# Performance work log

Hardware: AMD Instinct MI355X
Metric: run time of the kernel (lower is better)

The kernel has to match this reference:

```python
import jax, jax.numpy as jnp
import numpy as np


def setup_inputs() -> dict:
    key = jax.random.key(0)
    ks = jax.random.split(key, 7)
    B, S, D, F, E = 4, 2048, 1024, 4096, 8
    scale = 0.02
    return {
        "x": jax.random.normal(ks[0], (B, S, D), dtype=jnp.float32),
        "gate_w": jax.random.normal(ks[1], (D, E), dtype=jnp.float32) * scale,
        "gate_b": jnp.zeros((E,), dtype=jnp.float32),
        "w1": jax.random.normal(ks[2], (E, D, F), dtype=jnp.float32) * scale,
        "b1": jnp.zeros((E, F), dtype=jnp.float32),
        "w2": jax.random.normal(ks[3], (E, F, D), dtype=jnp.float32) * scale,
        "b2": jnp.zeros((E, D), dtype=jnp.float32),
        "top_k": 2,
    }


def reference(x, gate_w, gate_b, w1, b1, w2, b2, top_k):
    B, S, D = x.shape
    E = w1.shape[0]
    xf = x.reshape(-1, D)                      # [T, D], T = B*S
    T = xf.shape[0]

    # Router: top-k logits, softmax over the selected k (as in torch code)
    logits = xf @ gate_w + gate_b              # [T, E]
    rw, sel = jax.lax.top_k(logits, top_k)     # [T, k], [T, k]
    w = jax.nn.softmax(rw, axis=-1)            # [T, k]

    # Dense combine weights: combine[t, e] = sum_k w[t,k] * (sel[t,k]==e)
    combine = jnp.zeros((T, E), dtype=xf.dtype)
    combine = combine.at[jnp.arange(T)[:, None], sel].add(w)

    # Loop over small fixed expert count; each expert FFN on all tokens,
    # weighted by combine (zero for unrouted tokens). Dropout p honored as 0 (eval).
    out = jnp.zeros_like(xf)
    for e in range(E):
        h = jax.nn.gelu(xf @ w1[e] + b1[e], approximate=False)  # torch F.gelu = exact
        out = out + combine[:, e:e + 1] * (h @ w2[e] + b2[e])
    return out.reshape(B, S, D)
```

## Files before the change

### kernel.cpp

```cpp
#include <hip/hip_runtime.h>
#include <math.h>

#define T_TOK 8192
#define DDIM  1024
#define FDIM  4096
#define NEXP  8
#define MT256 72
#define NSLOT (2 * T_TOK)
#define NG1   (32 * MT256)
#define NG2   (16 * MT256)

typedef __attribute__((ext_vector_type(8))) short short8;
typedef __attribute__((ext_vector_type(4))) float f32x4;
typedef unsigned short u16;
typedef unsigned int   u32;

typedef const __attribute__((address_space(1))) u32* gp_t;
typedef       __attribute__((address_space(3))) u32* lp_t;

__device__ __forceinline__ void gload16(const void* g, void* l) {
  __builtin_amdgcn_global_load_lds((gp_t)g, (lp_t)l, 16, 0, 0);
}

#define VM0 asm volatile("s_waitcnt vmcnt(0)" ::: "memory")
#define SBAR __builtin_amdgcn_s_barrier()
#define SCHED0 __builtin_amdgcn_sched_barrier(0)

__device__ __forceinline__ u16 f2bf(float f) {
  u32 u = __float_as_uint(f);
  u = u + 0x7FFFu + ((u >> 16) & 1u);
  return (u16)(u >> 16);
}

__device__ __forceinline__ int imin(int a, int b) { return a < b ? a : b; }

__device__ __forceinline__ float gelu_fast(float v) {
  float u = 0.7978845608f * (v + 0.044715f * v * v * v);
  float t2 = __expf(2.f * u);
  float th = 1.f - 2.f / (t2 + 1.f);
  return 0.5f * v * (1.f + th);
}

__device__ __forceinline__ int xcd_swz(int orig, int nwg) {
  int xcd = orig & 7;
  int q = nwg >> 3, r = nwg & 7;
  int base = (xcd < r) ? xcd * (q + 1) : r * (q + 1) + (xcd - r) * q;
  return base + (orig >> 3);
}

__global__ __launch_bounds__(256) void router_kernel(
    const float* __restrict__ x, const float* __restrict__ gw,
    const float* __restrict__ gb,
    int* __restrict__ counts, int* __restrict__ sel, float* __restrict__ wts)
{
  const int t    = blockIdx.x * 4 + (threadIdx.x >> 6);
  const int lane = threadIdx.x & 63;
  const float* xr = x + (size_t)t * DDIM;
  float lg[NEXP];
  #pragma unroll
  for (int e = 0; e < NEXP; e++) lg[e] = 0.f;
  #pragma unroll
  for (int i = 0; i < 4; i++) {
    int d0 = i * 256 + lane * 4;
    float4 v = *(const float4*)(xr + d0);
    const float* g = gw + (size_t)d0 * NEXP;
    #pragma unroll
    for (int e = 0; e < NEXP; e++)
      lg[e] += v.x * g[e] + v.y * g[NEXP + e] + v.z * g[2 * NEXP + e] + v.w * g[3 * NEXP + e];
  }
  #pragma unroll
  for (int off = 32; off > 0; off >>= 1) {
    #pragma unroll
    for (int e = 0; e < NEXP; e++) lg[e] += __shfl_down(lg[e], off);
  }
  if (lane == 0) {
    float v0 = -1e30f, v1 = -1e30f; int s0 = 0, s1 = 0;
    #pragma unroll
    for (int e = 0; e < NEXP; e++) {
      float v = lg[e] + gb[e];
      if (v > v0) { v1 = v0; s1 = s0; v0 = v; s0 = e; }
      else if (v > v1) { v1 = v; s1 = e; }
    }
    float a  = expf(v1 - v0);
    float w0 = 1.f / (1.f + a);
    sel[t * 2] = s0; sel[t * 2 + 1] = s1;
    wts[t * 2] = w0; wts[t * 2 + 1] = 1.f - w0;
    atomicAdd(&counts[s0], 1); atomicAdd(&counts[s1], 1);
  }
}

__global__ __launch_bounds__(256) void scan_assign_kernel(
    const int* __restrict__ counts, const int* __restrict__ sel,
    const float* __restrict__ wts,
    int* __restrict__ offsets, int* __restrict__ map_e, int* __restrict__ map_r,
    int* __restrict__ nT, int* __restrict__ stok, float* __restrict__ swgt)
{
  __shared__ int spos[NEXP];
  if (threadIdx.x == 0) {
    int run = 0, nt = 0;
    for (int e = 0; e < NEXP; e++) {
      offsets[e] = run; spos[e] = run;
      int c = counts[e];
      int ntile = (c + 255) >> 8;
      for (int i = 0; i < ntile; i++) { map_e[nt] = e; map_r[nt] = i * 256; nt++; }
      run += c;
    }
    nT[0] = nt;
  }
  __syncthreads();
  for (int t = threadIdx.x; t < T_TOK; t += 256) {
    #pragma unroll
    for (int k = 0; k < 2; k++) {
      int e = sel[t * 2 + k];
      int p = atomicAdd(&spos[e], 1);
      stok[p] = t; swgt[p] = wts[t * 2 + k];
    }
  }
}

__global__ __launch_bounds__(256) void xgather_kernel(
    const float* __restrict__ x, const int* __restrict__ stok,
    u16* __restrict__ Xg)
{
  const int s = blockIdx.x;
  int tok = stok[s]; if ((u32)tok >= T_TOK) tok = 0;
  float4 v = *(const float4*)(x + (size_t)tok * DDIM + threadIdx.x * 4);
  ushort4 o;
  o.x = f2bf(v.x); o.y = f2bf(v.y); o.z = f2bf(v.z); o.w = f2bf(v.w);
  *(ushort4*)(Xg + (size_t)s * DDIM + threadIdx.x * 4) = o;
}

__device__ void wtrans_tile(float* __restrict__ tile,
                            const float* __restrict__ in, u16* __restrict__ out,
                            int M, int N, int r0, int c0)
{
  const int tid = threadIdx.x;
  const int tr = tid >> 4, tc = (tid & 15) * 4;
  #pragma unroll
  for (int p = 0; p < 4; p++) {
    int r = p * 16 + tr;
    float4 v = *(const float4*)(in + (size_t)(r0 + r) * N + (c0 + tc));
    tile[r * 65 + tc]     = v.x; tile[r * 65 + tc + 1] = v.y;
    tile[r * 65 + tc + 2] = v.z; tile[r * 65 + tc + 3] = v.w;
  }
  __syncthreads();
  const int oc = tid >> 3, om = (tid & 7) * 8;
  #pragma unroll
  for (int p = 0; p < 2; p++) {
    int c = p * 32 + oc;
    short8 o;
    #pragma unroll
    for (int j = 0; j < 8; j++) o[j] = (short)f2bf(tile[(om + j) * 65 + c]);
    *(short8*)(out + (size_t)(c0 + c) * M + (r0 + om)) = o;
  }
}

__global__ __launch_bounds__(256) void wtrans_all_kernel(
    const float* __restrict__ w1, u16* __restrict__ w1t,
    const float* __restrict__ w2, u16* __restrict__ w2t)
{
  __shared__ __align__(16) float tile[64 * 65];
  const int t = blockIdx.x;
  if (t < 8192) {
    int e = t >> 10, rem = t & 1023;
    int tm = rem >> 4, tn = rem & 15;
    wtrans_tile(tile, w2 + (size_t)e * FDIM * DDIM,
                w2t + (size_t)e * FDIM * DDIM, FDIM, DDIM, tm * 64, tn * 64);
  } else {
    int tt = t - 8192;
    int e = tt >> 10, rem = tt & 1023;
    int tn = rem >> 4, tm = rem & 15;
    wtrans_tile(tile, w1 + (size_t)e * DDIM * FDIM,
                w1t + (size_t)e * DDIM * FDIM, DDIM, FDIM, tm * 64, tn * 64);
  }
}

__global__ __launch_bounds__(512, 4) void gemm1_kernel(
    const u16* __restrict__ Xg, const u16* __restrict__ W1T,
    const float* __restrict__ B1,
    const int* __restrict__ counts, const int* __restrict__ offsets,
    const int* __restrict__ map_e, const int* __restrict__ map_r,
    const int* __restrict__ nT, u16* __restrict__ H)
{
  __shared__ __align__(16) char lds[2 * 24576];
  const int L     = xcd_swz(blockIdx.x, NG1);
  const int xg    = L / 288;
  const int local = L - xg * 288;
  const int tl    = local >> 5;
  const int n_idx = local & 31;
  const int t_idx = xg * 9 + tl;
  if (t_idx >= nT[0]) return;
  const int e    = map_e[t_idx];
  const int row0 = map_r[t_idx];
  const int cnt  = counts[e];
  const int off  = offsets[e];
  const int n0   = n_idx * 128;

  const int tid = threadIdx.x, wave = tid >> 6, lane = tid & 63;
  const int lr = lane & 15, lq = lane >> 4;
  const int wr = wave >> 1, wc = wave & 1;
  const int l2 = lane >> 2, lb = (lane & 3) * 16;

  const char* gA[2]; const char* gB;
  #pragma unroll
  for (int i = 0; i < 2; i++) {
    int R = (wave * 2 + i) * 16 + l2;
    int aidx = imin(off + row0 + R, NSLOT - 1);
    gA[i] = (const char*)Xg + (size_t)aidx * 2048 + lb;
  }
  {
    int R = wave * 16 + l2;
    gB = (const char*)W1T + (size_t)(e * FDIM + n0 + R) * 2048 + lb;
  }

  auto stage = [&](int buf, int k0) {
    char* base = lds + buf * 24576;
    gload16(gA[0] + k0, base + (wave * 2) * 1024 + lane * 16);
    gload16(gA[1] + k0, base + (wave * 2 + 1) * 1024 + lane * 16);
    gload16(gB + k0, base + 16384 + wave * 1024 + lane * 16);
  };

  f32x4 acc[4][4] = {};
  auto compute = [&](int buf) {
    const u16* As = (const u16*)(lds + buf * 24576);
    const u16* Bs = (const u16*)(lds + buf * 24576 + 16384);
    short8 a[4], bf[4];
    #pragma unroll
    for (int m = 0; m < 4; m++)
      a[m] = *(const short8*)&As[(wr * 64 + m * 16 + lr) * 32 + lq * 8];
    #pragma unroll
    for (int n = 0; n < 4; n++)
      bf[n] = *(const short8*)&Bs[(wc * 64 + n * 16 + lr) * 32 + lq * 8];
    #pragma unroll
    for (int m = 0; m < 4; m++)
      #pragma unroll
      for (int n = 0; n < 4; n++)
        acc[m][n] = __builtin_amdgcn_mfma_f32_16x16x32_bf16(a[m], bf[n], acc[m][n], 0, 0, 0);
  };

  stage(0, 0);
  VM0; SCHED0; SBAR; SCHED0;
  #pragma unroll 1
  for (int t = 0; t < 32; t++) {
    if (t < 31) stage((t + 1) & 1, (t + 1) * 64);
    compute(t & 1);
    SCHED0; VM0; SCHED0; SBAR; SCHED0;
  }

  #pragma unroll
  for (int nn = 0; nn < 4; nn++) {
    int col = n0 + wc * 64 + nn * 16 + lr;
    float b1v = B1[e * FDIM + col];
    #pragma unroll
    for (int m = 0; m < 4; m++) {
      int rbase = wr * 64 + m * 16 + lq * 4;
      #pragma unroll
      for (int j = 0; j < 4; j++) {
        int r = rbase + j;
        if (row0 + r < cnt) {
          float v = acc[m][nn][j] + b1v;
          H[(size_t)(off + row0 + r) * FDIM + col] = f2bf(gelu_fast(v));
        }
      }
    }
  }
}

__global__ __launch_bounds__(512, 4) void gemm2_kernel(
    const u16* __restrict__ H, const u16* __restrict__ W2T,
    const float* __restrict__ B2,
    const int* __restrict__ counts, const int* __restrict__ offsets,
    const int* __restrict__ slot_token, const float* __restrict__ slot_weight,
    const int* __restrict__ map_e, const int* __restrict__ map_r,
    const int* __restrict__ nT, float* __restrict__ out)
{
  __shared__ __align__(16) char lds[2 * 24576];
  const int L     = xcd_swz(blockIdx.x, NG2);
  const int xg    = L / 144;
  const int local = L - xg * 144;
  const int tl    = local >> 4;
  const int combo = local & 15;
  const int sp    = combo >> 3;
  const int n_idx = combo & 7;
  const int t_idx = xg * 9 + tl;
  if (t_idx >= nT[0]) return;
  const int e    = map_e[t_idx];
  const int row0 = map_r[t_idx];
  const int cnt  = counts[e];
  const int off  = offsets[e];
  const int n0   = n_idx * 128;
  const int kbase = sp * 4096;

  const int tid = threadIdx.x, wave = tid >> 6, lane = tid & 63;
  const int lr = lane & 15, lq = lane >> 4;
  const int wr = wave >> 1, wc = wave & 1;
  const int l2 = lane >> 2, lb = (lane & 3) * 16;

  const char* gA[2]; const char* gB;
  #pragma unroll
  for (int i = 0; i < 2; i++) {
    int R = (wave * 2 + i) * 16 + l2;
    int aidx = imin(off + row0 + R, NSLOT - 1);
    gA[i] = (const char*)H + (size_t)aidx * 8192 + kbase + lb;
  }
  {
    int R = wave * 16 + l2;
    gB = (const char*)W2T + (size_t)(e * DDIM + n0 + R) * 8192 + kbase + lb;
  }

  auto stage = [&](int buf, int k0) {
    char* base = lds + buf * 24576;
    gload16(gA[0] + k0, base + (wave * 2) * 1024 + lane * 16);
    gload16(gA[1] + k0, base + (wave * 2 + 1) * 1024 + lane * 16);
    gload16(gB + k0, base + 16384 + wave * 1024 + lane * 16);
  };

  f32x4 acc[4][4] = {};
  auto compute = [&](int buf) {
    const u16* As = (const u16*)(lds + buf * 24576);
    const u16* Bs = (const u16*)(lds + buf * 24576 + 16384);
    short8 a[4], bf[4];
    #pragma unroll
    for (int m = 0; m < 4; m++)
      a[m] = *(const short8*)&As[(wr * 64 + m * 16 + lr) * 32 + lq * 8];
    #pragma unroll
    for (int n = 0; n < 4; n++)
      bf[n] = *(const short8*)&Bs[(wc * 64 + n * 16 + lr) * 32 + lq * 8];
    #pragma unroll
    for (int m = 0; m < 4; m++)
      #pragma unroll
      for (int n = 0; n < 4; n++)
        acc[m][n] = __builtin_amdgcn_mfma_f32_16x16x32_bf16(a[m], bf[n], acc[m][n], 0, 0, 0);
  };

  stage(0, 0);
  VM0; SCHED0; SBAR; SCHED0;
  #pragma unroll 1
  for (int t = 0; t < 64; t++) {
    if (t < 63) stage((t + 1) & 1, (t + 1) * 64);
    compute(t & 1);
    SCHED0; VM0; SCHED0; SBAR; SCHED0;
  }

  #pragma unroll
  for (int m = 0; m < 4; m++) {
    int rbase = wr * 64 + m * 16 + lq * 4;
    #pragma unroll
    for (int j = 0; j < 4; j++) {
      int r = rbase + j;
      if (row0 + r >= cnt) continue;
      int s = off + row0 + r;
      int tok = slot_token[s];
      float wgt = slot_weight[s];
      #pragma unroll
      for (int n = 0; n < 4; n++) {
        int col = n0 + wc * 64 + n * 16 + lr;
        float v = acc[m][n][j];
        if (sp == 0) v += B2[e * DDIM + col];
        atomicAdd(&out[(size_t)tok * DDIM + col], wgt * v);
      }
    }
  }
}

extern "C" void kernel_launch(void* const* d_in, const int* in_sizes, int n_in,
                              void* d_out, int out_size, void* d_ws, size_t ws_size,
                              hipStream_t stream)
{
  (void)in_sizes; (void)n_in; (void)ws_size;
  const float* x  = (const float*)d_in[0];
  const float* gw = (const float*)d_in[1];
  const float* gb = (const float*)d_in[2];
  const float* w1 = (const float*)d_in[3];
  const float* b1 = (const float*)d_in[4];
  const float* w2 = (const float*)d_in[5];
  const float* b2 = (const float*)d_in[6];

  char* ws = (char*)d_ws;
  int*   counts = (int*)(ws + 0);
  int*   offp   = (int*)(ws + 64);
  int*   nT     = (int*)(ws + 128);
  int*   map_e  = (int*)(ws + 256);
  int*   map_r  = (int*)(ws + 1024);

  size_t p = 2048;
  int*   sel   = (int*)(ws + p);   p += (size_t)T_TOK * 2 * 4;
  float* wts   = (float*)(ws + p); p += (size_t)T_TOK * 2 * 4;
  int*   stok  = (int*)(ws + p);   p += (size_t)NSLOT * 4;
  float* swgt  = (float*)(ws + p); p += (size_t)NSLOT * 4;
  p = (p + 1048575) & ~(size_t)1048575;
  u16*   Xg    = (u16*)(ws + p);   p += (size_t)NSLOT * DDIM * 2;
  u16*   w1t   = (u16*)(ws + p);   p += (size_t)NEXP * DDIM * FDIM * 2;
  u16*   w2t   = (u16*)(ws + p);   p += (size_t)NEXP * DDIM * FDIM * 2;
  u16*   Hbuf  = (u16*)(ws + p);

  hipMemsetAsync(ws, 0, 256, stream);
  hipMemsetAsync(d_out, 0, (size_t)out_size * sizeof(float), stream);
  router_kernel<<<T_TOK / 4, 256, 0, stream>>>(x, gw, gb, counts, sel, wts);
  scan_assign_kernel<<<1, 256, 0, stream>>>(counts, sel, wts, offp, map_e, map_r, nT, stok, swgt);
  xgather_kernel<<<NSLOT, 256, 0, stream>>>(x, stok, Xg);
  wtrans_all_kernel<<<16384, 256, 0, stream>>>(w1, w1t, w2, w2t);
  gemm1_kernel<<<NG1, 512, 0, stream>>>(
      Xg, w1t, b1, counts, offp, map_e, map_r, nT, Hbuf);
  gemm2_kernel<<<NG2, 512, 0, stream>>>(
      Hbuf, w2t, b2, counts, offp, stok, swgt, map_e, map_r, nT, (float*)d_out);
}
```

Baseline: 870.0 us.

## Use 256x256 tiles with 16 waves and triple-buffered LDS pipeline in expert GEMMs

Both expert GEMM kernels now launch 1024-thread blocks (16 waves in a 4x4 arrangement) that compute 256-column output tiles, halving the grid size and improving operand reuse per block. The LDS staging moves from double to triple buffering with a prefetch distance of two K-steps, and uses vmcnt(2) waits so loads overlap compute further. In exchange, LDS use per block grows to 96KB and blocks are larger, which lowers occupancy and may leave CUs partly idle on tail tiles.

```diff
diff --git a/kernel.cpp b/kernel.cpp
--- a/kernel.cpp
+++ b/kernel.cpp
@@ -7,8 +7,8 @@
 #define NEXP  8
 #define MT256 72
 #define NSLOT (2 * T_TOK)
-#define NG1   (32 * MT256)
-#define NG2   (16 * MT256)
+#define NG1   (16 * MT256)
+#define NG2   (8 * MT256)
 
 typedef __attribute__((ext_vector_type(8))) short short8;
 typedef __attribute__((ext_vector_type(4))) float f32x4;
@@ -22,6 +22,7 @@
   __builtin_amdgcn_global_load_lds((gp_t)g, (lp_t)l, 16, 0, 0);
 }
 
+#define VM2 asm volatile("s_waitcnt vmcnt(2)" ::: "memory")
 #define VM0 asm volatile("s_waitcnt vmcnt(0)" ::: "memory")
 #define SBAR __builtin_amdgcn_s_barrier()
 #define SCHED0 __builtin_amdgcn_sched_barrier(0)
@@ -175,55 +176,47 @@
   }
 }
 
-__global__ __launch_bounds__(512, 4) void gemm1_kernel(
+__global__ __launch_bounds__(1024, 4) void gemm1_kernel(
     const u16* __restrict__ Xg, const u16* __restrict__ W1T,
     const float* __restrict__ B1,
     const int* __restrict__ counts, const int* __restrict__ offsets,
     const int* __restrict__ map_e, const int* __restrict__ map_r,
     const int* __restrict__ nT, u16* __restrict__ H)
 {
-  __shared__ __align__(16) char lds[2 * 24576];
+  __shared__ __align__(16) char lds[3 * 32768];
   const int L     = xcd_swz(blockIdx.x, NG1);
-  const int xg    = L / 288;
-  const int local = L - xg * 288;
-  const int tl    = local >> 5;
-  const int n_idx = local & 31;
+  const int xg    = L / 144;
+  const int local = L - xg * 144;
+  const int tl    = local >> 4;
+  const int n_idx = local & 15;
   const int t_idx = xg * 9 + tl;
   if (t_idx >= nT[0]) return;
   const int e    = map_e[t_idx];
   const int row0 = map_r[t_idx];
   const int cnt  = counts[e];
   const int off  = offsets[e];
-  const int n0   = n_idx * 128;
+  const int n0   = n_idx * 256;
 
   const int tid = threadIdx.x, wave = tid >> 6, lane = tid & 63;
   const int lr = lane & 15, lq = lane >> 4;
-  const int wr = wave >> 1, wc = wave & 1;
+  const int wr = wave >> 2, wc = wave & 3;
   const int l2 = lane >> 2, lb = (lane & 3) * 16;
 
-  const char* gA[2]; const char* gB;
-  #pragma unroll
-  for (int i = 0; i < 2; i++) {
-    int R = (wave * 2 + i) * 16 + l2;
-    int aidx = imin(off + row0 + R, NSLOT - 1);
-    gA[i] = (const char*)Xg + (size_t)aidx * 2048 + lb;
-  }
-  {
-    int R = wave * 16 + l2;
-    gB = (const char*)W1T + (size_t)(e * FDIM + n0 + R) * 2048 + lb;
-  }
-
-  auto stage = [&](int buf, int k0) {
-    char* base = lds + buf * 24576;
-    gload16(gA[0] + k0, base + (wave * 2) * 1024 + lane * 16);
-    gload16(gA[1] + k0, base + (wave * 2 + 1) * 1024 + lane * 16);
+  const int R = wave * 16 + l2;
+  int aidx = imin(off + row0 + R, NSLOT - 1);
+  const char* gA = (const char*)Xg + (size_t)aidx * 2048 + lb;
+  const char* gB = (const char*)W1T + (size_t)(e * FDIM + n0 + R) * 2048 + lb;
+
+  auto stage = [&](int slot, int k0) {
+    char* base = lds + slot * 32768;
+    gload16(gA + k0, base + wave * 1024 + lane * 16);
     gload16(gB + k0, base + 16384 + wave * 1024 + lane * 16);
   };
 
   f32x4 acc[4][4] = {};
-  auto compute = [&](int buf) {
-    const u16* As = (const u16*)(lds + buf * 24576);
-    const u16* Bs = (const u16*)(lds + buf * 24576 + 16384);
+  auto compute = [&](int slot) {
+    const u16* As = (const u16*)(lds + slot * 32768);
+    const u16* Bs = (const u16*)(lds + slot * 32768 + 16384);
     short8 a[4], bf[4];
     #pragma unroll
     for (int m = 0; m < 4; m++)
@@ -238,13 +231,16 @@
         acc[m][n] = __builtin_amdgcn_mfma_f32_16x16x32_bf16(a[m], bf[n], acc[m][n], 0, 0, 0);
   };
 
-  stage(0, 0);
-  VM0; SCHED0; SBAR; SCHED0;
+  stage(0, 0); stage(1, 64);
+  VM2; SCHED0; SBAR; SCHED0;
   #pragma unroll 1
   for (int t = 0; t < 32; t++) {
-    if (t < 31) stage((t + 1) & 1, (t + 1) * 64);
-    compute(t & 1);
-    SCHED0; VM0; SCHED0; SBAR; SCHED0;
+    if (t + 2 < 32) stage((t + 2) % 3, (t + 2) * 64);
+    compute(t % 3);
+    SCHED0;
+    if (t + 2 < 32)       { VM2; }
+    else if (t + 2 == 32) { VM0; }
+    SCHED0; SBAR; SCHED0;
   }
 
   #pragma unroll
@@ -266,7 +262,7 @@
   }
 }
 
-__global__ __launch_bounds__(512, 4) void gemm2_kernel(
+__global__ __launch_bounds__(1024, 4) void gemm2_kernel(
     const u16* __restrict__ H, const u16* __restrict__ W2T,
     const float* __restrict__ B2,
     const int* __restrict__ counts, const int* __restrict__ offsets,
@@ -274,51 +270,43 @@
     const int* __restrict__ map_e, const int* __restrict__ map_r,
     const int* __restrict__ nT, float* __restrict__ out)
 {
-  __shared__ __align__(16) char lds[2 * 24576];
+  __shared__ __align__(16) char lds[3 * 32768];
   const int L     = xcd_swz(blockIdx.x, NG2);
-  const int xg    = L / 144;
-  const int local = L - xg * 144;
-  const int tl    = local >> 4;
-  const int combo = local & 15;
-  const int sp    = combo >> 3;
-  const int n_idx = combo & 7;
+  const int xg    = L / 72;
+  const int local = L - xg * 72;
+  const int tl    = local >> 3;
+  const int combo = local & 7;
+  const int sp    = combo >> 2;
+  const int n_idx = combo & 3;
   const int t_idx = xg * 9 + tl;
   if (t_idx >= nT[0]) return;
   const int e    = map_e[t_idx];
   const int row0 = map_r[t_idx];
   const int cnt  = counts[e];
   const int off  = offsets[e];
-  const int n0   = n_idx * 128;
+  const int n0   = n_idx * 256;
   const int kbase = sp * 4096;
 
   const int tid = threadIdx.x, wave = tid >> 6, lane = tid & 63;
   const int lr = lane & 15, lq = lane >> 4;
-  const int wr = wave >> 1, wc = wave & 1;
+  const int wr = wave >> 2, wc = wave & 3;
   const int l2 = lane >> 2, lb = (lane & 3) * 16;
 
-  const char* gA[2]; const char* gB;
-  #pragma unroll
-  for (int i = 0; i < 2; i++) {
-    int R = (wave * 2 + i) * 16 + l2;
-    int aidx = imin(off + row0 + R, NSLOT - 1);
-    gA[i] = (const char*)H + (size_t)aidx * 8192 + kbase + lb;
-  }
-  {
-    int R = wave * 16 + l2;
-    gB = (const char*)W2T + (size_t)(e * DDIM + n0 + R) * 8192 + kbase + lb;
-  }
-
-  auto stage = [&](int buf, int k0) {
-    char* base = lds + buf * 24576;
-    gload16(gA[0] + k0, base + (wave * 2) * 1024 + lane * 16);
-    gload16(gA[1] + k0, base + (wave * 2 + 1) * 1024 + lane * 16);
+  const int R = wave * 16 + l2;
+  int aidx = imin(off + row0 + R, NSLOT - 1);
+  const char* gA = (const char*)H + (size_t)aidx * 8192 + kbase + lb;
+  const char* gB = (const char*)W2T + (size_t)(e * DDIM + n0 + R) * 8192 + kbase + lb;
+
+  auto stage = [&](int slot, int k0) {
+    char* base = lds + slot * 32768;
+    gload16(gA + k0, base + wave * 1024 + lane * 16);
     gload16(gB + k0, base + 16384 + wave * 1024 + lane * 16);
   };
 
   f32x4 acc[4][4] = {};
-  auto compute = [&](int buf) {
-    const u16* As = (const u16*)(lds + buf * 24576);
-    const u16* Bs = (const u16*)(lds + buf * 24576 + 16384);
+  auto compute = [&](int slot) {
+    const u16* As = (const u16*)(lds + slot * 32768);
+    const u16* Bs = (const u16*)(lds + slot * 32768 + 16384);
     short8 a[4], bf[4];
     #pragma unroll
     for (int m = 0; m < 4; m++)
@@ -333,13 +321,16 @@
         acc[m][n] = __builtin_amdgcn_mfma_f32_16x16x32_bf16(a[m], bf[n], acc[m][n], 0, 0, 0);
   };
 
-  stage(0, 0);
-  VM0; SCHED0; SBAR; SCHED0;
+  stage(0, 0); stage(1, 64);
+  VM2; SCHED0; SBAR; SCHED0;
   #pragma unroll 1
   for (int t = 0; t < 64; t++) {
-    if (t < 63) stage((t + 1) & 1, (t + 1) * 64);
-    compute(t & 1);
-    SCHED0; VM0; SCHED0; SBAR; SCHED0;
+    if (t + 2 < 64) stage((t + 2) % 3, (t + 2) * 64);
+    compute(t % 3);
+    SCHED0;
+    if (t + 2 < 64)       { VM2; }
+    else if (t + 2 == 64) { VM0; }
+    SCHED0; SBAR; SCHED0;
   }
 
   #pragma unroll
@@ -400,8 +391,8 @@
   scan_assign_kernel<<<1, 256, 0, stream>>>(counts, sel, wts, offp, map_e, map_r, nT, stok, swgt);
   xgather_kernel<<<NSLOT, 256, 0, stream>>>(x, stok, Xg);
   wtrans_all_kernel<<<16384, 256, 0, stream>>>(w1, w1t, w2, w2t);
-  gemm1_kernel<<<NG1, 512, 0, stream>>>(
+  gemm1_kernel<<<NG1, 1024, 0, stream>>>(
       Xg, w1t, b1, counts, offp, map_e, map_r, nT, Hbuf);
-  gemm2_kernel<<<NG2, 512, 0, stream>>>(
+  gemm2_kernel<<<NG2, 1024, 0, stream>>>(
       Hbuf, w2t, b2, counts, offp, stok, swgt, map_e, map_r, nT, (float*)d_out);
 }
```

Result: faster. 834.4 us (-4.1%).
